# Kernel optimization log

Hardware: AMD Instinct MI355X
Metric: run time of the kernel (lower is better)

The kernel has to match this reference:

```python
import jax, jax.numpy as jnp
import numpy as np

N = 64       # number of nodes (features)
K = 512      # sequence length
WIN = 5
KS = 5       # conv kernel size
EMBED = 64   # embed_dim


def setup_inputs() -> dict:
    key = jax.random.key(0)
    ks = jax.random.split(key, 8)
    x = jax.random.normal(ks[0], (N, K), dtype=jnp.float32)
    # fully connected graph without self loops (remove_self_loops is then a no-op)
    src, dst = np.nonzero(~np.eye(N, dtype=bool))
    edge_index = jnp.asarray(np.stack([src, dst]), dtype=jnp.int32)  # [2, E]
    conv_w = jax.random.normal(ks[1], (1, 1, KS), dtype=jnp.float32) * 0.3
    conv_b = jnp.zeros((1,), jnp.float32)
    s = 1.0 / np.sqrt(WIN)
    lin_l_w = jax.random.uniform(ks[2], (EMBED, WIN), jnp.float32, -s, s)
    lin_l_b = jax.random.uniform(ks[3], (EMBED,), jnp.float32, -s, s)
    lin_r_w = jax.random.uniform(ks[4], (EMBED, WIN), jnp.float32, -s, s)
    lin_r_b = jax.random.uniform(ks[5], (EMBED,), jnp.float32, -s, s)
    glorot = np.sqrt(6.0 / (1 + EMBED))
    att = jax.random.uniform(ks[6], (1, EMBED), jnp.float32, -glorot, glorot)
    return dict(x=x, edge_index=edge_index, conv_w=conv_w, conv_b=conv_b,
                lin_l_w=lin_l_w, lin_l_b=lin_l_b, lin_r_w=lin_r_w,
                lin_r_b=lin_r_b, att=att)


def reference(x, edge_index, conv_w, conv_b, lin_l_w, lin_l_b, lin_r_w, lin_r_b, att):
    n_temp = K - WIN + 1
    # Conv1d(1,1,KS, padding='same') + sigmoid
    h = jax.lax.conv_general_dilated(x[:, None, :], conv_w, window_strides=(1,),
                                     padding='SAME',
                                     dimension_numbers=('NCH', 'OIH', 'NCH'))
    h = jax.nn.sigmoid(h[:, 0, :] + conv_b)                      # [N, K]
    widx = jnp.arange(n_temp)[:, None] + jnp.arange(WIN)[None, :]
    xw = h[:, widx].reshape(-1, WIN)
    # temporal edge index: node idx -> idx*n_temp + t
    t = jnp.arange(n_temp)[None, :]
    l = (edge_index[0][:, None] * n_temp + t).reshape(-1)        # [E*n_temp]
    r = (edge_index[1][:, None] * n_temp + t).reshape(-1)
    x_l = xw @ lin_l_w.T + lin_l_b                               # [N*n_temp, EMBED]
    x_r = xw @ lin_r_w.T + lin_r_b
    e = jax.nn.leaky_relu(x_l[l] + x_r[r], negative_slope=0.2)   # [E*n_temp, EMBED]
    alpha = (e * att).sum(-1)                                    # [E*n_temp]
    # segment softmax grouped by source temporal node l
    S = N * n_temp
    m = jax.ops.segment_max(alpha, l, num_segments=S)
    a = jnp.exp(alpha - m[l])
    denom = jax.ops.segment_sum(a, l, num_segments=S)
    alpha = a / (denom[l] + 1e-16)
    return alpha.reshape(-1, n_temp)                             # [E, n_temp]
```

## Files before the change

### kernel.cpp

```cpp
#include <hip/hip_runtime.h>

#define NNODE 64
#define KLEN  512
#define WIN   5
#define NT    508
#define EMB   64
#define NDST  63
#define XRP   68

__device__ __forceinline__ float readlane_f(float v, int l) {
    return __int_as_float(__builtin_amdgcn_readlane(__float_as_int(v), l));
}

__global__ __launch_bounds__(256) void attn_fused(
    const float* __restrict__ x,
    const float* __restrict__ conv_w,
    const float* __restrict__ conv_b,
    const float* __restrict__ lin_l_w,
    const float* __restrict__ lin_l_b,
    const float* __restrict__ lin_r_w,
    const float* __restrict__ lin_r_b,
    const float* __restrict__ att,
    float* __restrict__ out)
{
    const int bx = blockIdx.x;
    const int t  = (bx & 7) * 64 + (bx >> 3);
    if (t >= NT) return;
    const int sg   = blockIdx.y;
    const int tid  = threadIdx.x;
    const int lane = tid & 63;
    const int wave = tid >> 6;

    __shared__ float h_s[NNODE][8];
    __shared__ float xr_s[NNODE][XRP];

    for (int idx = tid; idx < NNODE * WIN; idx += 256) {
        const int n = idx / WIN;
        const int w = idx % WIN;
        const int base = t + w - 2;
        float acc = conv_b[0];
        #pragma unroll
        for (int j = 0; j < WIN; ++j) {
            const int k = base + j;
            const float xv = (k >= 0 && k < KLEN) ? x[n * KLEN + k] : 0.f;
            acc = fmaf(conv_w[j], xv, acc);
        }
        h_s[n][w] = 1.f / (1.f + __expf(-acc));
    }
    __syncthreads();

    const float attv = att[lane];

    {
        float rw[WIN];
        #pragma unroll
        for (int w = 0; w < WIN; ++w) rw[w] = lin_r_w[lane * WIN + w];
        const float rb = lin_r_b[lane];
        #pragma unroll
        for (int k = 0; k < 16; ++k) {
            const int r = wave + k * 4;
            float acc = rb;
            #pragma unroll
            for (int w = 0; w < WIN; ++w)
                acc = fmaf(rw[w], h_s[r][w], acc);
            xr_s[r][lane] = acc;
        }
    }

    float xlv[4], A[4];
    {
        float lw[WIN];
        #pragma unroll
        for (int w = 0; w < WIN; ++w) lw[w] = lin_l_w[lane * WIN + w];
        const float lb = lin_l_b[lane];
        #pragma unroll
        for (int p = 0; p < 4; ++p) {
            const int s = sg * 16 + wave * 4 + p;
            float acc = lb;
            #pragma unroll
            for (int w = 0; w < WIN; ++w)
                acc = fmaf(lw[w], h_s[s][w], acc);
            xlv[p] = acc;
            float v = attv * acc;
            #pragma unroll
            for (int off = 32; off; off >>= 1) v += __shfl_xor(v, off);
            A[p] = v;
        }
    }
    __syncthreads();

    float accm[4] = {0.f, 0.f, 0.f, 0.f};
    float accB = 0.f;
    const float* xrrow = &xr_s[lane][0];
    #pragma unroll
    for (int d0 = 0; d0 < EMB; d0 += 4) {
        const float4 xr4 = *(const float4*)(xrrow + d0);
        const float a0 = att[d0 + 0];
        const float a1 = att[d0 + 1];
        const float a2 = att[d0 + 2];
        const float a3 = att[d0 + 3];
        accB = fmaf(a0, xr4.x, accB);
        accB = fmaf(a1, xr4.y, accB);
        accB = fmaf(a2, xr4.z, accB);
        accB = fmaf(a3, xr4.w, accB);
        #pragma unroll
        for (int p = 0; p < 4; ++p) {
            float z;
            z = readlane_f(xlv[p], d0 + 0) + xr4.x;
            accm[p] = fmaf(a0, fminf(z, 0.f), accm[p]);
            z = readlane_f(xlv[p], d0 + 1) + xr4.y;
            accm[p] = fmaf(a1, fminf(z, 0.f), accm[p]);
            z = readlane_f(xlv[p], d0 + 2) + xr4.z;
            accm[p] = fmaf(a2, fminf(z, 0.f), accm[p]);
            z = readlane_f(xlv[p], d0 + 3) + xr4.w;
            accm[p] = fmaf(a3, fminf(z, 0.f), accm[p]);
        }
    }

    #pragma unroll
    for (int p = 0; p < 4; ++p) {
        const int s = sg * 16 + wave * 4 + p;
        float alpha = fmaf(-0.8f, accm[p], A[p] + accB);
        if (lane == s) alpha = -INFINITY;
        float m = alpha;
        #pragma unroll
        for (int off = 32; off; off >>= 1) m = fmaxf(m, __shfl_xor(m, off));
        float ex = __expf(alpha - m);
        if (lane == s) ex = 0.f;
        float sum = ex;
        #pragma unroll
        for (int off = 32; off; off >>= 1) sum += __shfl_xor(sum, off);
        const float res = ex / (sum + 1e-16f);
        if (lane != s) {
            const int j = lane - (lane > s ? 1 : 0);
            const int e = s * NDST + j;
            out[(size_t)e * NT + t] = res;
        }
    }
}

extern "C" void kernel_launch(void* const* d_in, const int* in_sizes, int n_in,
                              void* d_out, int out_size, void* d_ws, size_t ws_size,
                              hipStream_t stream)
{
    const float* x       = (const float*)d_in[0];
    const float* conv_w  = (const float*)d_in[2];
    const float* conv_b  = (const float*)d_in[3];
    const float* lin_l_w = (const float*)d_in[4];
    const float* lin_l_b = (const float*)d_in[5];
    const float* lin_r_w = (const float*)d_in[6];
    const float* lin_r_b = (const float*)d_in[7];
    const float* att     = (const float*)d_in[8];
    float* out = (float*)d_out;

    attn_fused<<<dim3(512, 4), 256, 0, stream>>>(x, conv_w, conv_b,
        lin_l_w, lin_l_b, lin_r_w, lin_r_b, att, out);
}
```

Measured before the change: 34.73 us.

## Split into precompute kernel writing projections to workspace, use abs-form leaky ReLU

Adds a first kernel that computes the conv, sigmoid and both linear projections once per time step and writes x_l, x_r and the attention dot terms A and B to workspace. This removes the fourth-fold recomputation across the four source-group blocks. The main kernel then loads x_r into shared memory and reads x_l from global memory with wave-uniform addresses instead of using readlane. Leaky ReLU is rewritten as 0.6*z + 0.4*|z|, which folds the linear part into precomputed A+B terms. In exchange it adds a second launch and roughly 17 MB of workspace traffic each way.

```diff
diff --git a/kernel.cpp b/kernel.cpp
--- a/kernel.cpp
+++ b/kernel.cpp
@@ -8,11 +8,13 @@
 #define NDST  63
 #define XRP   68
 
-__device__ __forceinline__ float readlane_f(float v, int l) {
-    return __int_as_float(__builtin_amdgcn_readlane(__float_as_int(v), l));
-}
-
-__global__ __launch_bounds__(256) void attn_fused(
+#define XL_OFF 0
+#define XR_OFF ((size_t)NT * NNODE * EMB)
+#define A_OFF  ((size_t)2 * NT * NNODE * EMB)
+#define B_OFF  (A_OFF + (size_t)NT * NNODE)
+#define WS_FLOATS (B_OFF + (size_t)NT * NNODE)
+
+__global__ __launch_bounds__(256) void precompute_k(
     const float* __restrict__ x,
     const float* __restrict__ conv_w,
     const float* __restrict__ conv_b,
@@ -20,6 +22,89 @@
     const float* __restrict__ lin_l_b,
     const float* __restrict__ lin_r_w,
     const float* __restrict__ lin_r_b,
+    const float* __restrict__ att,
+    float* __restrict__ ws)
+{
+    const int bx = blockIdx.x;
+    const int t  = (bx & 7) * 64 + (bx >> 3);
+    if (t >= NT) return;
+    const int tid  = threadIdx.x;
+    const int lane = tid & 63;
+    const int wave = tid >> 6;
+
+    __shared__ float h_s[NNODE][9];
+
+    for (int idx = tid; idx < NNODE * WIN; idx += 256) {
+        const int n = idx / WIN;
+        const int w = idx % WIN;
+        const int base = t + w - 2;
+        float acc = conv_b[0];
+        #pragma unroll
+        for (int j = 0; j < WIN; ++j) {
+            const int k = base + j;
+            const float xv = (k >= 0 && k < KLEN) ? x[n * KLEN + k] : 0.f;
+            acc = fmaf(conv_w[j], xv, acc);
+        }
+        h_s[n][w] = 1.f / (1.f + __expf(-acc));
+    }
+    __syncthreads();
+
+    float* xl_ws = ws + XL_OFF + (size_t)t * NNODE * EMB;
+    float* xr_ws = ws + XR_OFF + (size_t)t * NNODE * EMB;
+
+    {
+        float lw[WIN], rw[WIN];
+        #pragma unroll
+        for (int w = 0; w < WIN; ++w) {
+            lw[w] = lin_l_w[lane * WIN + w];
+            rw[w] = lin_r_w[lane * WIN + w];
+        }
+        const float lb = lin_l_b[lane];
+        const float rb = lin_r_b[lane];
+        #pragma unroll
+        for (int k = 0; k < 16; ++k) {
+            const int n = wave + 4 * k;
+            float xl = lb, xr = rb;
+            #pragma unroll
+            for (int w = 0; w < WIN; ++w) {
+                const float hv = h_s[n][w];
+                xl = fmaf(lw[w], hv, xl);
+                xr = fmaf(rw[w], hv, xr);
+            }
+            xl_ws[n * EMB + lane] = xl;
+            xr_ws[n * EMB + lane] = xr;
+        }
+    }
+
+    if (wave < 2) {
+        const float attv = att[lane];
+        const float* W = (wave == 0) ? lin_l_w : lin_r_w;
+        const float* Bv = (wave == 0) ? lin_l_b : lin_r_b;
+        float c[WIN], c0;
+        #pragma unroll
+        for (int w = 0; w < WIN; ++w) {
+            float v = attv * W[lane * WIN + w];
+            #pragma unroll
+            for (int off = 32; off; off >>= 1) v += __shfl_xor(v, off);
+            c[w] = v;
+        }
+        {
+            float v = attv * Bv[lane];
+            #pragma unroll
+            for (int off = 32; off; off >>= 1) v += __shfl_xor(v, off);
+            c0 = v;
+        }
+        float acc = c0;
+        #pragma unroll
+        for (int w = 0; w < WIN; ++w)
+            acc = fmaf(c[w], h_s[lane][w], acc);
+        float* AB = ws + (wave == 0 ? A_OFF : B_OFF) + (size_t)t * NNODE;
+        AB[lane] = acc;
+    }
+}
+
+__global__ __launch_bounds__(256) void attn_main(
+    const float* __restrict__ ws,
     const float* __restrict__ att,
     float* __restrict__ out)
 {
@@ -31,66 +116,28 @@
     const int lane = tid & 63;
     const int wave = tid >> 6;
 
-    __shared__ float h_s[NNODE][8];
     __shared__ float xr_s[NNODE][XRP];
 
-    for (int idx = tid; idx < NNODE * WIN; idx += 256) {
-        const int n = idx / WIN;
-        const int w = idx % WIN;
-        const int base = t + w - 2;
-        float acc = conv_b[0];
-        #pragma unroll
-        for (int j = 0; j < WIN; ++j) {
-            const int k = base + j;
-            const float xv = (k >= 0 && k < KLEN) ? x[n * KLEN + k] : 0.f;
-            acc = fmaf(conv_w[j], xv, acc);
-        }
-        h_s[n][w] = 1.f / (1.f + __expf(-acc));
-    }
+    {
+        const float* xr_g = ws + XR_OFF + (size_t)t * NNODE * EMB;
+        #pragma unroll
+        for (int rr = 0; rr < 4; ++rr) {
+            const int idx = rr * 1024 + tid * 4;
+            const float4 v = *(const float4*)(xr_g + idx);
+            *(float4*)(&xr_s[idx >> 6][idx & 63]) = v;
+        }
+    }
+
+    const float Bl = ws[B_OFF + (size_t)t * NNODE + lane];
+
+    const int wu = __builtin_amdgcn_readfirstlane(wave);
+    const int s0 = sg * 16 + wu * 4;
+    const float* xl_g = ws + XL_OFF + (size_t)t * NNODE * EMB + (size_t)s0 * EMB;
+    const float* A_g  = ws + A_OFF + (size_t)t * NNODE + s0;
+
     __syncthreads();
 
-    const float attv = att[lane];
-
-    {
-        float rw[WIN];
-        #pragma unroll
-        for (int w = 0; w < WIN; ++w) rw[w] = lin_r_w[lane * WIN + w];
-        const float rb = lin_r_b[lane];
-        #pragma unroll
-        for (int k = 0; k < 16; ++k) {
-            const int r = wave + k * 4;
-            float acc = rb;
-            #pragma unroll
-            for (int w = 0; w < WIN; ++w)
-                acc = fmaf(rw[w], h_s[r][w], acc);
-            xr_s[r][lane] = acc;
-        }
-    }
-
-    float xlv[4], A[4];
-    {
-        float lw[WIN];
-        #pragma unroll
-        for (int w = 0; w < WIN; ++w) lw[w] = lin_l_w[lane * WIN + w];
-        const float lb = lin_l_b[lane];
-        #pragma unroll
-        for (int p = 0; p < 4; ++p) {
-            const int s = sg * 16 + wave * 4 + p;
-            float acc = lb;
-            #pragma unroll
-            for (int w = 0; w < WIN; ++w)
-                acc = fmaf(lw[w], h_s[s][w], acc);
-            xlv[p] = acc;
-            float v = attv * acc;
-            #pragma unroll
-            for (int off = 32; off; off >>= 1) v += __shfl_xor(v, off);
-            A[p] = v;
-        }
-    }
-    __syncthreads();
-
     float accm[4] = {0.f, 0.f, 0.f, 0.f};
-    float accB = 0.f;
     const float* xrrow = &xr_s[lane][0];
     #pragma unroll
     for (int d0 = 0; d0 < EMB; d0 += 4) {
@@ -99,28 +146,21 @@
         const float a1 = att[d0 + 1];
         const float a2 = att[d0 + 2];
         const float a3 = att[d0 + 3];
-        accB = fmaf(a0, xr4.x, accB);
-        accB = fmaf(a1, xr4.y, accB);
-        accB = fmaf(a2, xr4.z, accB);
-        accB = fmaf(a3, xr4.w, accB);
         #pragma unroll
         for (int p = 0; p < 4; ++p) {
+            const float* xlp = xl_g + p * EMB + d0;
             float z;
-            z = readlane_f(xlv[p], d0 + 0) + xr4.x;
-            accm[p] = fmaf(a0, fminf(z, 0.f), accm[p]);
-            z = readlane_f(xlv[p], d0 + 1) + xr4.y;
-            accm[p] = fmaf(a1, fminf(z, 0.f), accm[p]);
-            z = readlane_f(xlv[p], d0 + 2) + xr4.z;
-            accm[p] = fmaf(a2, fminf(z, 0.f), accm[p]);
-            z = readlane_f(xlv[p], d0 + 3) + xr4.w;
-            accm[p] = fmaf(a3, fminf(z, 0.f), accm[p]);
+            z = xlp[0] + xr4.x; accm[p] = fmaf(a0, fabsf(z), accm[p]);
+            z = xlp[1] + xr4.y; accm[p] = fmaf(a1, fabsf(z), accm[p]);
+            z = xlp[2] + xr4.z; accm[p] = fmaf(a2, fabsf(z), accm[p]);
+            z = xlp[3] + xr4.w; accm[p] = fmaf(a3, fabsf(z), accm[p]);
         }
     }
 
     #pragma unroll
     for (int p = 0; p < 4; ++p) {
-        const int s = sg * 16 + wave * 4 + p;
-        float alpha = fmaf(-0.8f, accm[p], A[p] + accB);
+        const int s = s0 + p;
+        float alpha = fmaf(0.4f, accm[p], 0.6f * (A_g[p] + Bl));
         if (lane == s) alpha = -INFINITY;
         float m = alpha;
         #pragma unroll
@@ -152,7 +192,9 @@
     const float* lin_r_b = (const float*)d_in[7];
     const float* att     = (const float*)d_in[8];
     float* out = (float*)d_out;
-
-    attn_fused<<<dim3(512, 4), 256, 0, stream>>>(x, conv_w, conv_b,
-        lin_l_w, lin_l_b, lin_r_w, lin_r_b, att, out);
+    float* ws  = (float*)d_ws;
+
+    precompute_k<<<dim3(512), 256, 0, stream>>>(x, conv_w, conv_b,
+        lin_l_w, lin_l_b, lin_r_w, lin_r_b, att, ws);
+    attn_main<<<dim3(512, 4), 256, 0, stream>>>(ws, att, out);
 }
```

Result: faster. 29.41 us (-15.3%).

## Split into alpha kernel plus tiled transpose for coalesced output writes

Applied to the files above, without the earlier changes.

The fused kernel now writes each softmax row to a workspace laid out by time step. A second kernel then transposes 64x64 tiles through shared memory, so the scattered writes strided by NT become coalesced stores to the [E, NT] output. The alpha kernel also changes: each lane computes its own x_r row in registers, leaky_relu is rewritten as 0.6z + 0.4|z|, the softmax max-subtraction is dropped, and a single block covers all 64 sources. The cost is an extra launch, a round trip through an 8 MB workspace, and heavy register use. Removing the max-subtraction relies on alpha staying bounded, which the sigmoid inputs make likely.

```diff
diff --git a/kernel.cpp b/kernel.cpp
--- a/kernel.cpp
+++ b/kernel.cpp
@@ -6,13 +6,13 @@
 #define NT    508
 #define EMB   64
 #define NDST  63
-#define XRP   68
+#define WSROW 4096
 
 __device__ __forceinline__ float readlane_f(float v, int l) {
     return __int_as_float(__builtin_amdgcn_readlane(__float_as_int(v), l));
 }
 
-__global__ __launch_bounds__(256) void attn_fused(
+__global__ __launch_bounds__(256) void fused_alpha(
     const float* __restrict__ x,
     const float* __restrict__ conv_w,
     const float* __restrict__ conv_b,
@@ -21,18 +21,16 @@
     const float* __restrict__ lin_r_w,
     const float* __restrict__ lin_r_b,
     const float* __restrict__ att,
-    float* __restrict__ out)
+    float* __restrict__ ws)
 {
     const int bx = blockIdx.x;
     const int t  = (bx & 7) * 64 + (bx >> 3);
     if (t >= NT) return;
-    const int sg   = blockIdx.y;
     const int tid  = threadIdx.x;
     const int lane = tid & 63;
     const int wave = tid >> 6;
 
-    __shared__ float h_s[NNODE][8];
-    __shared__ float xr_s[NNODE][XRP];
+    __shared__ float h_s[NNODE][9];
 
     for (int idx = tid; idx < NNODE * WIN; idx += 256) {
         const int n = idx / WIN;
@@ -49,92 +47,101 @@
     }
     __syncthreads();
 
-    const float attv = att[lane];
+    float hl[WIN];
+    #pragma unroll
+    for (int w = 0; w < WIN; ++w) hl[w] = h_s[lane][w];
 
-    {
-        float rw[WIN];
+    float xrr[EMB];
+    #pragma unroll
+    for (int d = 0; d < EMB; ++d) {
+        float acc = lin_r_b[d];
         #pragma unroll
-        for (int w = 0; w < WIN; ++w) rw[w] = lin_r_w[lane * WIN + w];
-        const float rb = lin_r_b[lane];
+        for (int w = 0; w < WIN; ++w)
+            acc = fmaf(lin_r_w[d * WIN + w], hl[w], acc);
+        xrr[d] = acc;
+    }
+    float Bp0 = 0.f, Bp1 = 0.f, Bp2 = 0.f, Bp3 = 0.f;
+    #pragma unroll
+    for (int d = 0; d < EMB; d += 4) {
+        Bp0 = fmaf(att[d + 0], xrr[d + 0], Bp0);
+        Bp1 = fmaf(att[d + 1], xrr[d + 1], Bp1);
+        Bp2 = fmaf(att[d + 2], xrr[d + 2], Bp2);
+        Bp3 = fmaf(att[d + 3], xrr[d + 3], Bp3);
+    }
+    const float Bl = (Bp0 + Bp1) + (Bp2 + Bp3);
+
+    float llw[WIN];
+    #pragma unroll
+    for (int w = 0; w < WIN; ++w) llw[w] = lin_l_w[lane * WIN + w];
+    const float llb  = lin_l_b[lane];
+    const float attl = att[lane];
+    float xlv[16], A[16];
+    #pragma unroll
+    for (int i = 0; i < 16; ++i) {
+        const int s = wave * 16 + i;
+        float acc = llb;
         #pragma unroll
-        for (int k = 0; k < 16; ++k) {
-            const int r = wave + k * 4;
-            float acc = rb;
-            #pragma unroll
-            for (int w = 0; w < WIN; ++w)
-                acc = fmaf(rw[w], h_s[r][w], acc);
-            xr_s[r][lane] = acc;
-        }
+        for (int w = 0; w < WIN; ++w)
+            acc = fmaf(llw[w], h_s[s][w], acc);
+        xlv[i] = acc;
+        float v = attl * acc;
+        #pragma unroll
+        for (int off = 32; off; off >>= 1) v += __shfl_xor(v, off);
+        A[i] = v;
     }
 
-    float xlv[4], A[4];
-    {
-        float lw[WIN];
+    float* wrow = ws + (size_t)t * WSROW + (size_t)(wave * 16) * 64 + lane;
+    #pragma unroll
+    for (int i = 0; i < 16; ++i) {
+        const int s = wave * 16 + i;
+        float p0 = 0.f, p1 = 0.f, p2 = 0.f, p3 = 0.f;
         #pragma unroll
-        for (int w = 0; w < WIN; ++w) lw[w] = lin_l_w[lane * WIN + w];
-        const float lb = lin_l_b[lane];
-        #pragma unroll
-        for (int p = 0; p < 4; ++p) {
-            const int s = sg * 16 + wave * 4 + p;
-            float acc = lb;
-            #pragma unroll
-            for (int w = 0; w < WIN; ++w)
-                acc = fmaf(lw[w], h_s[s][w], acc);
-            xlv[p] = acc;
-            float v = attv * acc;
-            #pragma unroll
-            for (int off = 32; off; off >>= 1) v += __shfl_xor(v, off);
-            A[p] = v;
+        for (int d = 0; d < EMB; d += 4) {
+            const float z0 = readlane_f(xlv[i], d + 0) + xrr[d + 0];
+            p0 = fmaf(att[d + 0], fabsf(z0), p0);
+            const float z1 = readlane_f(xlv[i], d + 1) + xrr[d + 1];
+            p1 = fmaf(att[d + 1], fabsf(z1), p1);
+            const float z2 = readlane_f(xlv[i], d + 2) + xrr[d + 2];
+            p2 = fmaf(att[d + 2], fabsf(z2), p2);
+            const float z3 = readlane_f(xlv[i], d + 3) + xrr[d + 3];
+            p3 = fmaf(att[d + 3], fabsf(z3), p3);
         }
-    }
-    __syncthreads();
-
-    float accm[4] = {0.f, 0.f, 0.f, 0.f};
-    float accB = 0.f;
-    const float* xrrow = &xr_s[lane][0];
-    #pragma unroll
-    for (int d0 = 0; d0 < EMB; d0 += 4) {
-        const float4 xr4 = *(const float4*)(xrrow + d0);
-        const float a0 = att[d0 + 0];
-        const float a1 = att[d0 + 1];
-        const float a2 = att[d0 + 2];
-        const float a3 = att[d0 + 3];
-        accB = fmaf(a0, xr4.x, accB);
-        accB = fmaf(a1, xr4.y, accB);
-        accB = fmaf(a2, xr4.z, accB);
-        accB = fmaf(a3, xr4.w, accB);
-        #pragma unroll
-        for (int p = 0; p < 4; ++p) {
-            float z;
-            z = readlane_f(xlv[p], d0 + 0) + xr4.x;
-            accm[p] = fmaf(a0, fminf(z, 0.f), accm[p]);
-            z = readlane_f(xlv[p], d0 + 1) + xr4.y;
-            accm[p] = fmaf(a1, fminf(z, 0.f), accm[p]);
-            z = readlane_f(xlv[p], d0 + 2) + xr4.z;
-            accm[p] = fmaf(a2, fminf(z, 0.f), accm[p]);
-            z = readlane_f(xlv[p], d0 + 3) + xr4.w;
-            accm[p] = fmaf(a3, fminf(z, 0.f), accm[p]);
-        }
-    }
-
-    #pragma unroll
-    for (int p = 0; p < 4; ++p) {
-        const int s = sg * 16 + wave * 4 + p;
-        float alpha = fmaf(-0.8f, accm[p], A[p] + accB);
-        if (lane == s) alpha = -INFINITY;
-        float m = alpha;
-        #pragma unroll
-        for (int off = 32; off; off >>= 1) m = fmaxf(m, __shfl_xor(m, off));
-        float ex = __expf(alpha - m);
-        if (lane == s) ex = 0.f;
+        const float alpha = fmaf(0.4f, (p0 + p1) + (p2 + p3),
+                                 0.6f * (A[i] + Bl));
+        float ex = (lane == s) ? 0.f : __expf(alpha);
         float sum = ex;
         #pragma unroll
         for (int off = 32; off; off >>= 1) sum += __shfl_xor(sum, off);
-        const float res = ex / (sum + 1e-16f);
-        if (lane != s) {
-            const int j = lane - (lane > s ? 1 : 0);
-            const int e = s * NDST + j;
-            out[(size_t)e * NT + t] = res;
+        const float res = ex * __builtin_amdgcn_rcpf(sum + 1e-16f);
+        wrow[i * 64] = res;
+    }
+}
+
+__global__ __launch_bounds__(256) void transpose_norm(
+    const float* __restrict__ ws,
+    float* __restrict__ out)
+{
+    const int bx = blockIdx.x;
+    const int tt = bx & 7;
+    const int s  = bx >> 3;
+    const int t0 = tt * 64;
+    const int tid  = threadIdx.x;
+    const int lane = tid & 63;
+    const int wave = tid >> 6;
+
+    __shared__ float tile[64][65];
+
+    const float* src = ws + (size_t)t0 * WSROW + (size_t)s * 64;
+    #pragma unroll
+    for (int i = wave; i < 64; i += 4)
+        tile[i][lane] = src[(size_t)i * WSROW + lane];
+    __syncthreads();
+
+    const int tcol = t0 + lane;
+    if (tcol < NT) {
+        for (int j = wave; j < NDST; j += 4) {
+            const int r = j + (j >= s ? 1 : 0);
+            out[(size_t)(s * NDST + j) * NT + tcol] = tile[lane][r];
         }
     }
 }
@@ -152,7 +159,9 @@
     const float* lin_r_b = (const float*)d_in[7];
     const float* att     = (const float*)d_in[8];
     float* out = (float*)d_out;
+    float* ws  = (float*)d_ws;
 
-    attn_fused<<<dim3(512, 4), 256, 0, stream>>>(x, conv_w, conv_b,
-        lin_l_w, lin_l_b, lin_r_w, lin_r_b, att, out);
+    fused_alpha<<<dim3(512), 256, 0, stream>>>(x, conv_w, conv_b,
+        lin_l_w, lin_l_b, lin_r_w, lin_r_b, att, ws);
+    transpose_norm<<<dim3(512), 256, 0, stream>>>(ws, out);
 }
```

Result: slower. 46.24 us (+33.1%).
